# Performance work log

Measured on AMD Instinct MI355X. Metric: run time of the kernel, lower is better.

The kernel has to match this reference:

```python
import jax, jax.numpy as jnp
import numpy as np

DIM = 1024
NUM_HEADS = 8
HEAD_DIM = 128
MAX_SEQ_LEN = 2048
ATTN_SCALE = 0.12
RMS_EPS = 1.1920929e-07  # torch float32 eps (F.rms_norm default)


def rms_norm(x):
    return x * jax.lax.rsqrt(jnp.mean(jnp.square(x), axis=-1, keepdims=True) + RMS_EPS)


def rope_tables(T):
    # angular_freq: (1/1024)**linspace(0,1,head_dim//4), padded with head_dim//4 zeros -> length head_dim//2
    af = (1.0 / 1024.0) ** np.linspace(0.0, 1.0, HEAD_DIM // 4, dtype=np.float32)
    af = np.concatenate([af, np.zeros(HEAD_DIM // 4, dtype=np.float32)])
    t = np.arange(T, dtype=np.float32)
    theta = np.einsum('i,j->ij', t, af)  # [T, head_dim//2]
    return jnp.asarray(np.cos(theta)), jnp.asarray(np.sin(theta))


def apply_rope(x_BTHD, cos, sin):
    # cos/sin: [T, head_dim//2] -> broadcast [1,T,1,hd//2]
    c = cos[None, :, None, :]
    s = sin[None, :, None, :]
    x1, x2 = jnp.split(x_BTHD, 2, axis=-1)
    y1 = x1 * c + x2 * s
    y2 = -x1 * s + x2 * c
    return jnp.concatenate([y1, y2], axis=-1)


def setup_inputs() -> dict:
    key = jax.random.key(0)
    k1, k2, k3, k4, k5 = jax.random.split(key, 5)
    B, T = 4, 2048
    hdim = NUM_HEADS * HEAD_DIM
    std = 0.5 * DIM ** (-0.5)
    bound = (3.0 ** 0.5) * std
    x = jax.random.normal(k1, (B, T, DIM), dtype=jnp.float32)
    ve = jax.random.normal(k2, (B, T, DIM), dtype=jnp.float32)
    sa_lambdas = jax.random.uniform(k3, (2,), dtype=jnp.float32)
    qkv_w = jax.random.uniform(k4, (3, hdim, DIM), dtype=jnp.float32, minval=-bound, maxval=bound)
    # original inits c_proj to zeros; use small random so the output is non-trivial
    c_proj_weight = jax.random.normal(k5, (DIM, hdim), dtype=jnp.float32) * 0.02
    return {"x": x, "ve": ve, "sa_lambdas": sa_lambdas, "qkv_w": qkv_w,
            "c_proj_weight": c_proj_weight}


def reference(x, ve, sa_lambdas, qkv_w, c_proj_weight):
    B, T, D = x.shape
    H, hd = NUM_HEADS, HEAD_DIM
    Wqkv = qkv_w.reshape(3 * H * hd, D)
    qkv = jnp.einsum('btd,ed->bte', x, Wqkv).reshape(B, T, 3 * H, hd)
    q, k, v = jnp.split(qkv, 3, axis=-2)  # each [B,T,H,hd]
    q, k = rms_norm(q), rms_norm(k)
    cos, sin = rope_tables(T)
    q, k = apply_rope(q, cos, sin), apply_rope(k, cos, sin)
    v = sa_lambdas[0] * v + sa_lambdas[1] * ve.reshape(B, T, H, hd)
    # [B,H,T,T] scores
    attn = jnp.einsum('bqhd,bkhd->bhqk', q, k) * ATTN_SCALE
    causal = jnp.triu(jnp.ones((T, T), dtype=bool), k=1)
    attn = jnp.where(causal[None, None], -jnp.inf, attn)
    attn = jax.nn.softmax(attn, axis=-1)
    y = jnp.einsum('bhqk,bkhd->bqhd', attn, v).reshape(B, T, H * hd)
    return jnp.einsum('bte,de->btd', y, c_proj_weight)
```

## Files before the change

kernel.cpp:

```cpp
#include <hip/hip_runtime.h>

#define DIM 1024
#define NH 8
#define HD 128
#define T_SEQ 2048
#define NTOK 8192
#define QKV_N 3072
#define ATTN_SCALE 0.12f
#define RMS_EPS 1.1920929e-07f

using f32x4  = __attribute__((ext_vector_type(4))) float;
using bf16x8 = __attribute__((ext_vector_type(8))) __bf16;

__device__ __forceinline__ unsigned short f2bf(float f) {
    unsigned int u = __builtin_bit_cast(unsigned int, f);
    u += 0x7fffu + ((u >> 16) & 1u);
    return (unsigned short)(u >> 16);
}
__device__ __forceinline__ float bf2f(unsigned short s) {
    unsigned int u = ((unsigned int)s) << 16;
    return __builtin_bit_cast(float, u);
}
__device__ __forceinline__ unsigned int cvtpk(float lo, float hi) {
    unsigned int r;
    asm("v_cvt_pk_bf16_f32 %0, %1, %2" : "=v"(r) : "v"(lo), "v"(hi));
    return r;
}

__device__ __forceinline__ void gll16(const void* g, void* l) {
    __builtin_amdgcn_global_load_lds(
        (const __attribute__((address_space(1))) unsigned int*)g,
        (__attribute__((address_space(3))) unsigned int*)l, 16, 0, 0);
}

#define VMCNT(n) asm volatile("s_waitcnt vmcnt(" #n ")" ::: "memory")

__global__ __launch_bounds__(256) void cvt_f32_bf16(const float* __restrict__ in,
                                                    unsigned short* __restrict__ out,
                                                    int n4) {
    int i = blockIdx.x * 256 + threadIdx.x;
    if (i < n4) {
        float4 f = ((const float4*)in)[i];
        ushort4 o;
        o.x = f2bf(f.x); o.y = f2bf(f.y); o.z = f2bf(f.z); o.w = f2bf(f.w);
        ((ushort4*)out)[i] = o;
    }
}

__global__ __launch_bounds__(256) void rope_tab(float2* __restrict__ tab) {
    int idx = blockIdx.x * 256 + threadIdx.x;
    int t = idx >> 5, i = idx & 31;
    float th = (float)t * exp2f((float)i * (-10.0f/31.0f));
    float sn, cs;
    sincosf(th, &sn, &cs);
    tab[idx] = make_float2(cs, sn);
}

#define SLOT_A 32768
#define SLOT_SZ 49152

template<int OUTF32>
__global__ __launch_bounds__(512, 1) void gemm256(const unsigned short* __restrict__ A,
                                                  const unsigned short* __restrict__ B,
                                                  void* __restrict__ Cout,
                                                  int M, int N, int K, int nbn) {
    __shared__ __align__(16) char smem[147456];
    const int tid  = threadIdx.x;
    const int lane = tid & 63;
    const int w    = tid >> 6;
    const int wm   = w >> 1, wn = w & 1;
    const int lr   = lane & 15, lg = lane >> 4;
    const int xsw  = (lr & 7) << 3;

    const int chunk = gridDim.x >> 3;
    const int bid2  = (blockIdx.x & 7) * chunk + (blockIdx.x >> 3);
    const int m0 = (bid2 / nbn) * 256;
    const int n0 = (bid2 % nbn) * 128;

    const int rsub = lane >> 3;
    const int csw  = ((lane & 7) ^ rsub) << 3;

    char* s0 = smem;
    char* s1 = smem + SLOT_SZ;
    char* s2 = smem + 2*SLOT_SZ;

    auto stage = [&](int kt, char* slot) {
        const int kb = kt * 64;
        #pragma unroll
        for (int i = 0; i < 4; ++i) {
            int c = w*4 + i;
            gll16(&A[(size_t)(m0 + c*8 + rsub)*K + kb + csw], slot + c*1024);
        }
        #pragma unroll
        for (int i = 0; i < 2; ++i) {
            int c = w*2 + i;
            gll16(&B[(size_t)(n0 + c*8 + rsub)*K + kb + csw], slot + SLOT_A + c*1024);
        }
    };

    f32x4 acc[4][4] = {};
    const int KT = K / 64;

    stage(0, s0);
    stage(1, s1);
    VMCNT(6);
    __builtin_amdgcn_s_barrier();
    __builtin_amdgcn_sched_barrier(0);

    for (int t = 0; t < KT; ++t) {
        if (t + 2 < KT) stage(t + 2, s2);
        const unsigned short* sA = (const unsigned short*)s0;
        const unsigned short* sB = (const unsigned short*)(s0 + SLOT_A);
        bf16x8 bfr[4][2];
        #pragma unroll
        for (int n = 0; n < 4; ++n)
            #pragma unroll
            for (int kk = 0; kk < 2; ++kk)
                bfr[n][kk] = *(const bf16x8*)&sB[(wn*64 + n*16 + lr)*64 + ((kk*32 + lg*8) ^ xsw)];
        #pragma unroll
        for (int m = 0; m < 4; ++m) {
            bf16x8 af[2];
            #pragma unroll
            for (int kk = 0; kk < 2; ++kk)
                af[kk] = *(const bf16x8*)&sA[(wm*64 + m*16 + lr)*64 + ((kk*32 + lg*8) ^ xsw)];
            __builtin_amdgcn_s_setprio(1);
            #pragma unroll
            for (int n = 0; n < 4; ++n)
                #pragma unroll
                for (int kk = 0; kk < 2; ++kk)
                    acc[m][n] = __builtin_amdgcn_mfma_f32_16x16x32_bf16(af[kk], bfr[n][kk], acc[m][n], 0, 0, 0);
            __builtin_amdgcn_s_setprio(0);
        }
        if (t + 2 < KT) { VMCNT(6); }
        else            { VMCNT(0); }
        __builtin_amdgcn_s_barrier();
        __builtin_amdgcn_sched_barrier(0);
        char* tmp = s0; s0 = s1; s1 = s2; s2 = tmp;
    }

    __syncthreads();
    float* sc = (float*)(smem + (size_t)w * 17408);
    #pragma unroll
    for (int m = 0; m < 4; ++m)
        #pragma unroll
        for (int n = 0; n < 4; ++n)
            #pragma unroll
            for (int r = 0; r < 4; ++r)
                sc[(m*16 + lg*4 + r)*68 + n*16 + lr] = acc[m][n][r];

    if (OUTF32) {
        float* C = (float*)Cout;
        #pragma unroll
        for (int rnd = 0; rnd < 16; ++rnd) {
            int g = rnd*64 + lane;
            int row = g >> 4, c4 = (g & 15) * 4;
            float4 v = *(float4*)&sc[row*68 + c4];
            *(float4*)&C[(size_t)(m0 + wm*64 + row)*N + n0 + wn*64 + c4] = v;
        }
    } else {
        unsigned short* C = (unsigned short*)Cout;
        #pragma unroll
        for (int rnd = 0; rnd < 8; ++rnd) {
            int g = rnd*64 + lane;
            int row = g >> 3, c8 = (g & 7) * 8;
            float4 v0 = *(float4*)&sc[row*68 + c8];
            float4 v1 = *(float4*)&sc[row*68 + c8 + 4];
            uint4 o;
            o.x = f2bf(v0.x) | ((unsigned)f2bf(v0.y) << 16);
            o.y = f2bf(v0.z) | ((unsigned)f2bf(v0.w) << 16);
            o.z = f2bf(v1.x) | ((unsigned)f2bf(v1.y) << 16);
            o.w = f2bf(v1.z) | ((unsigned)f2bf(v1.w) << 16);
            *(uint4*)&C[(size_t)(m0 + wm*64 + row)*N + n0 + wn*64 + c8] = o;
        }
    }
}

__global__ __launch_bounds__(256) void qkv_post(const unsigned short* __restrict__ qkv,
                                                const float2* __restrict__ tab,
                                                unsigned short* __restrict__ qO,
                                                unsigned short* __restrict__ kO) {
    int gw   = (blockIdx.x * 256 + threadIdx.x) >> 6;
    int lane = threadIdx.x & 63;
    int h     = gw & 7;
    int token = gw >> 3;
    int t     = token & (T_SEQ-1);
    int b     = token >> 11;

    const unsigned short* base = qkv + (size_t)token * QKV_N + h*HD;
    float q1 = bf2f(base[lane]),        q2 = bf2f(base[lane+64]);
    float k1 = bf2f(base[1024+lane]),   k2 = bf2f(base[1024+lane+64]);

    float sq = q1*q1 + q2*q2;
    float sk = k1*k1 + k2*k2;
    #pragma unroll
    for (int m = 1; m < 64; m <<= 1) {
        sq += __shfl_xor(sq, m);
        sk += __shfl_xor(sk, m);
    }
    float qs = rsqrtf(sq * (1.0f/128.0f) + RMS_EPS) * (ATTN_SCALE * 1.44269504088896f);
    float ks = rsqrtf(sk * (1.0f/128.0f) + RMS_EPS);
    q1 *= qs; q2 *= qs; k1 *= ks; k2 *= ks;

    float cs = 1.0f, sn = 0.0f;
    if (lane < 32) { float2 cc = tab[t*32 + lane]; cs = cc.x; sn = cc.y; }
    float qy1 =  q1*cs + q2*sn, qy2 = -q1*sn + q2*cs;
    float ky1 =  k1*cs + k2*sn, ky2 = -k1*sn + k2*cs;

    size_t obase = ((size_t)(b*NH + h) * T_SEQ + t) * HD;
    qO[obase + lane]      = f2bf(qy1);
    qO[obase + lane + 64] = f2bf(qy2);
    kO[obase + lane]      = f2bf(ky1);
    kO[obase + lane + 64] = f2bf(ky2);
}

__global__ __launch_bounds__(256) void vmix_t(const unsigned short* __restrict__ qkv,
                                              const float* __restrict__ ve,
                                              const float* __restrict__ lam,
                                              unsigned short* __restrict__ vt) {
    __shared__ unsigned short lT[128*72];
    const int tid = threadIdx.x;
    const int t0  = blockIdx.x * 64;
    const int bh  = blockIdx.y;
    const int b = bh >> 3, h = bh & 7;
    const float l0 = lam[0], l1 = lam[1];

    #pragma unroll
    for (int it = 0; it < 4; ++it) {
        int g  = it*256 + tid;
        int t  = g >> 4;
        int d8 = (g & 15) << 3;
        size_t token = (size_t)b*T_SEQ + t0 + t;
        ushort4 v0 = *(const ushort4*)&qkv[token*QKV_N + 2048 + h*HD + d8];
        ushort4 v1 = *(const ushort4*)&qkv[token*QKV_N + 2048 + h*HD + d8 + 4];
        float4 e0 = *(const float4*)&ve[token*DIM + h*HD + d8];
        float4 e1 = *(const float4*)&ve[token*DIM + h*HD + d8 + 4];
        lT[(d8+0)*72 + t] = f2bf(l0*bf2f(v0.x) + l1*e0.x);
        lT[(d8+1)*72 + t] = f2bf(l0*bf2f(v0.y) + l1*e0.y);
        lT[(d8+2)*72 + t] = f2bf(l0*bf2f(v0.z) + l1*e0.z);
        lT[(d8+3)*72 + t] = f2bf(l0*bf2f(v0.w) + l1*e0.w);
        lT[(d8+4)*72 + t] = f2bf(l0*bf2f(v1.x) + l1*e1.x);
        lT[(d8+5)*72 + t] = f2bf(l0*bf2f(v1.y) + l1*e1.y);
        lT[(d8+6)*72 + t] = f2bf(l0*bf2f(v1.z) + l1*e1.z);
        lT[(d8+7)*72 + t] = f2bf(l0*bf2f(v1.w) + l1*e1.w);
    }
    __syncthreads();
    #pragma unroll
    for (int it = 0; it < 4; ++it) {
        int g  = it*256 + tid;
        int d  = g >> 3;
        int t8 = (g & 7) << 3;
        uint4 pk = *(const uint4*)&lT[d*72 + t8];
        *(uint4*)&vt[((size_t)bh*HD + d)*T_SEQ + t0 + t8] = pk;
    }
}

__global__ __launch_bounds__(256, 2) void attn_fwd(const unsigned short* __restrict__ Q,
                                                   const unsigned short* __restrict__ K,
                                                   const unsigned short* __restrict__ Vt,
                                                   unsigned short* __restrict__ Y) {
    __shared__ unsigned short lK[2][64*128];
    __shared__ unsigned short lV[2][128*64];
    __shared__ unsigned short lP[4][16*72];
    __shared__ float lden[4][2][16];

    const int tid  = threadIdx.x;
    const int lane = tid & 63;
    const int w    = tid >> 6;
    const int lr   = lane & 15, lg = lane >> 4;

    const int lin = blockIdx.y * 16 + blockIdx.x;
    const int bh  = (lin & 7)*4 + ((lin >> 3) & 3);
    const int p   = lin >> 5;
    const int qtA = p, qtB = 31 - p;

    const unsigned short* Qg = Q  + (size_t)bh * T_SEQ * HD;
    const unsigned short* Kg = K  + (size_t)bh * T_SEQ * HD;
    const unsigned short* Vg = Vt + (size_t)bh * HD * T_SEQ;
    const int q0A = qtA*64 + w*16;
    const int q0B = qtB*64 + w*16;

    auto stage = [&](int kt, int s) {
        const int kbase = kt * 64;
        #pragma unroll
        for (int i = 0; i < 4; ++i) {
            int c = w*4 + i;
            int row = c*4 + (lane >> 4);
            int col = ((lane & 15) << 3) ^ ((row & 7) << 3);
            gll16(&Kg[(size_t)(kbase + row)*HD + col], &lK[s][c*512]);
        }
        #pragma unroll
        for (int i = 0; i < 4; ++i) {
            int c = w*4 + i;
            int row = c*8 + (lane >> 3);
            int col = ((lane & 7) << 3) ^ ((row & 7) << 3);
            gll16(&Vg[(size_t)row*T_SEQ + kbase + col], &lV[s][c*512]);
        }
    };

    bf16x8 qfA[4], qfB[4];
    #pragma unroll
    for (int kk = 0; kk < 4; ++kk) {
        qfA[kk] = *(const bf16x8*)&Qg[(size_t)(q0A + lr)*HD + kk*32 + lg*8];
        qfB[kk] = *(const bf16x8*)&Qg[(size_t)(q0B + lr)*HD + kk*32 + lg*8];
    }
    VMCNT(0);
    #pragma unroll
    for (int kk = 0; kk < 4; ++kk)
        asm volatile("" :: "v"(qfA[kk]), "v"(qfB[kk]));

    f32x4 oA[8] = {}, oB[8] = {};
    float psA = 0.f, psB = 0.f;

    auto pass = [&](const bf16x8* qf, f32x4* o, float& ps, int q0, bool diag,
                    int kbase, const unsigned short* lKc, const unsigned short* lVc) {
        f32x4 sf[4];
        __builtin_amdgcn_s_setprio(1);
        #pragma unroll
        for (int j = 0; j < 4; ++j) {
            f32x4 s = {0.f,0.f,0.f,0.f};
            #pragma unroll
            for (int kk = 0; kk < 4; ++kk) {
                bf16x8 kf = *(const bf16x8*)&lKc[(j*16+lr)*128 + ((kk*32 + lg*8) ^ ((lr&7)<<3))];
                s = __builtin_amdgcn_mfma_f32_16x16x32_bf16(kf, qf[kk], s, 0, 0, 0);
            }
            sf[j] = s;
        }
        __builtin_amdgcn_s_setprio(0);
        if (diag) {
            #pragma unroll
            for (int j = 0; j < 4; ++j)
                #pragma unroll
                for (int r = 0; r < 4; ++r) {
                    int kcol = kbase + j*16 + lg*4 + r;
                    int qrow = q0 + lr;
                    if (kcol > qrow) sf[j][r] = -INFINITY;
                }
        }
        #pragma unroll
        for (int j = 0; j < 4; ++j)
            #pragma unroll
            for (int r = 0; r < 4; ++r) {
                float pp = exp2f(sf[j][r]);
                sf[j][r] = pp;
                ps += pp;
            }
        asm volatile("" ::: "memory");
        #pragma unroll
        for (int j = 0; j < 4; ++j) {
            uint2 pk;
            pk.x = cvtpk(sf[j][0], sf[j][1]);
            pk.y = cvtpk(sf[j][2], sf[j][3]);
            *(uint2*)&lP[w][lr*72 + j*16 + lg*4] = pk;
        }
        asm volatile("" ::: "memory");
        bf16x8 pf[2];
        #pragma unroll
        for (int kk = 0; kk < 2; ++kk)
            pf[kk] = *(const bf16x8*)&lP[w][lr*72 + kk*32 + lg*8];
        #pragma unroll
        for (int n = 0; n < 8; ++n) {
            bf16x8 vf0 = *(const bf16x8*)&lVc[(n*16+lr)*64 + (( 0 + lg*8) ^ ((lr&7)<<3))];
            bf16x8 vf1 = *(const bf16x8*)&lVc[(n*16+lr)*64 + ((32 + lg*8) ^ ((lr&7)<<3))];
            __builtin_amdgcn_s_setprio(1);
            o[n] = __builtin_amdgcn_mfma_f32_16x16x32_bf16(pf[0], vf0, o[n], 0, 0, 0);
            o[n] = __builtin_amdgcn_mfma_f32_16x16x32_bf16(pf[1], vf1, o[n], 0, 0, 0);
            __builtin_amdgcn_s_setprio(0);
        }
    };

    stage(0, 0);
    for (int kt = 0; kt <= qtB; ++kt) {
        __builtin_amdgcn_s_barrier();
        const bool pre = (kt + 1 <= qtB);
        if (pre) stage(kt + 1, (kt + 1) & 1);
        if (pre) { VMCNT(8); } else { VMCNT(0); }
        __builtin_amdgcn_sched_barrier(0);
        const int kbase = kt * 64;
        const unsigned short* lKc = lK[kt & 1];
        const unsigned short* lVc = lV[kt & 1];
        if (kt <= qtA) pass(qfA, oA, psA, q0A, kt == qtA, kbase, lKc, lVc);
        pass(qfB, oB, psB, q0B, kt == qtB, kbase, lKc, lVc);
    }

    psA += __shfl_xor(psA, 16); psA += __shfl_xor(psA, 32);
    psB += __shfl_xor(psB, 16); psB += __shfl_xor(psB, 32);
    if (lane < 16) { lden[w][0][lane] = psA; lden[w][1][lane] = psB; }
    asm volatile("" ::: "memory");
    float riA[4], riB[4];
    #pragma unroll
    for (int r = 0; r < 4; ++r) {
        riA[r] = 1.0f / lden[w][0][lg*4 + r];
        riB[r] = 1.0f / lden[w][1][lg*4 + r];
    }

    const int b = bh >> 3, h = bh & 7;
    #pragma unroll
    for (int n = 0; n < 8; ++n)
        #pragma unroll
        for (int r = 0; r < 4; ++r) {
            int d = n*16 + lr;
            int qrowA = q0A + lg*4 + r;
            int qrowB = q0B + lg*4 + r;
            Y[((size_t)(b*T_SEQ + qrowA))*DIM + h*HD + d] = f2bf(oA[n][r] * riA[r]);
            Y[((size_t)(b*T_SEQ + qrowB))*DIM + h*HD + d] = f2bf(oB[n][r] * riB[r]);
        }
}

extern "C" void kernel_launch(void* const* d_in, const int* in_sizes, int n_in,
                              void* d_out, int out_size, void* d_ws, size_t ws_size,
                              hipStream_t stream) {
    const float* x      = (const float*)d_in[0];
    const float* ve     = (const float*)d_in[1];
    const float* lam    = (const float*)d_in[2];
    const float* qkvw   = (const float*)d_in[3];
    const float* cprojw = (const float*)d_in[4];

    char* ws = (char*)d_ws;
    unsigned short* xb  = (unsigned short*)(ws);
    unsigned short* wqb = (unsigned short*)(ws + 16777216);
    unsigned short* cpb = (unsigned short*)(ws + 23068672);
    unsigned short* qkv = (unsigned short*)(ws + 25165824);
    unsigned short* qa  = (unsigned short*)(ws + 75497472);
    unsigned short* ka  = (unsigned short*)(ws + 92274688);
    unsigned short* vt  = (unsigned short*)(ws + 109051904);
    unsigned short* ya  = (unsigned short*)(ws + 125829120);
    float2* tab = (float2*)(ws);

    cvt_f32_bf16<<<8192, 256, 0, stream>>>(x, xb, 2097152);
    cvt_f32_bf16<<<3072, 256, 0, stream>>>(qkvw, wqb, 786432);
    cvt_f32_bf16<<<1024, 256, 0, stream>>>(cprojw, cpb, 262144);

    gemm256<0><<<768, 512, 0, stream>>>(xb, wqb, qkv, NTOK, QKV_N, DIM, 24);
    rope_tab<<<256, 256, 0, stream>>>(tab);
    qkv_post<<<16384, 256, 0, stream>>>(qkv, tab, qa, ka);
    vmix_t<<<dim3(32, 32), 256, 0, stream>>>(qkv, ve, lam, vt);
    attn_fwd<<<dim3(16, 32), 256, 0, stream>>>(qa, ka, vt, ya);
    gemm256<1><<<256, 512, 0, stream>>>(ya, cpb, (float*)d_out, NTOK, DIM, DIM, 8);
}
```

Baseline: 199.5 us.

## Merge prep kernels into one launch and share K/V fragments across two query tiles

```diff
diff --git a/kernel.cpp b/kernel.cpp
--- a/kernel.cpp
+++ b/kernel.cpp
@@ -35,25 +35,34 @@
 
 #define VMCNT(n) asm volatile("s_waitcnt vmcnt(" #n ")" ::: "memory")
 
-__global__ __launch_bounds__(256) void cvt_f32_bf16(const float* __restrict__ in,
-                                                    unsigned short* __restrict__ out,
-                                                    int n4) {
-    int i = blockIdx.x * 256 + threadIdx.x;
-    if (i < n4) {
+__global__ __launch_bounds__(256) void prep(const float* __restrict__ x,
+                                            const float* __restrict__ qkvw,
+                                            const float* __restrict__ cprojw,
+                                            unsigned short* __restrict__ xb,
+                                            unsigned short* __restrict__ wqb,
+                                            unsigned short* __restrict__ cpb,
+                                            float2* __restrict__ tab) {
+    const int bid = blockIdx.x;
+    const int tid = threadIdx.x;
+    if (bid < 12288) {
+        const float* in;
+        unsigned short* out;
+        int i;
+        if (bid < 8192)        { in = x;      out = xb;  i = bid*256 + tid; }
+        else if (bid < 11264)  { in = qkvw;   out = wqb; i = (bid-8192)*256 + tid; }
+        else                   { in = cprojw; out = cpb; i = (bid-11264)*256 + tid; }
         float4 f = ((const float4*)in)[i];
         ushort4 o;
         o.x = f2bf(f.x); o.y = f2bf(f.y); o.z = f2bf(f.z); o.w = f2bf(f.w);
         ((ushort4*)out)[i] = o;
-    }
-}
-
-__global__ __launch_bounds__(256) void rope_tab(float2* __restrict__ tab) {
-    int idx = blockIdx.x * 256 + threadIdx.x;
-    int t = idx >> 5, i = idx & 31;
-    float th = (float)t * exp2f((float)i * (-10.0f/31.0f));
-    float sn, cs;
-    sincosf(th, &sn, &cs);
-    tab[idx] = make_float2(cs, sn);
+    } else {
+        int idx = (bid - 12288)*256 + tid;
+        int t = idx >> 5, i = idx & 31;
+        float th = (float)t * exp2f((float)i * (-10.0f/31.0f));
+        float sn, cs;
+        sincosf(th, &sn, &cs);
+        tab[idx] = make_float2(cs, sn);
+    }
 }
 
 #define SLOT_A 32768
@@ -311,31 +320,7 @@
     f32x4 oA[8] = {}, oB[8] = {};
     float psA = 0.f, psB = 0.f;
 
-    auto pass = [&](const bf16x8* qf, f32x4* o, float& ps, int q0, bool diag,
-                    int kbase, const unsigned short* lKc, const unsigned short* lVc) {
-        f32x4 sf[4];
-        __builtin_amdgcn_s_setprio(1);
-        #pragma unroll
-        for (int j = 0; j < 4; ++j) {
-            f32x4 s = {0.f,0.f,0.f,0.f};
-            #pragma unroll
-            for (int kk = 0; kk < 4; ++kk) {
-                bf16x8 kf = *(const bf16x8*)&lKc[(j*16+lr)*128 + ((kk*32 + lg*8) ^ ((lr&7)<<3))];
-                s = __builtin_amdgcn_mfma_f32_16x16x32_bf16(kf, qf[kk], s, 0, 0, 0);
-            }
-            sf[j] = s;
-        }
-        __builtin_amdgcn_s_setprio(0);
-        if (diag) {
-            #pragma unroll
-            for (int j = 0; j < 4; ++j)
-                #pragma unroll
-                for (int r = 0; r < 4; ++r) {
-                    int kcol = kbase + j*16 + lg*4 + r;
-                    int qrow = q0 + lr;
-                    if (kcol > qrow) sf[j][r] = -INFINITY;
-                }
-        }
+    auto softmax_store = [&](f32x4* sf, float& ps) {
         #pragma unroll
         for (int j = 0; j < 4; ++j)
             #pragma unroll
@@ -344,7 +329,6 @@
                 sf[j][r] = pp;
                 ps += pp;
             }
-        asm volatile("" ::: "memory");
         #pragma unroll
         for (int j = 0; j < 4; ++j) {
             uint2 pk;
@@ -353,17 +337,95 @@
             *(uint2*)&lP[w][lr*72 + j*16 + lg*4] = pk;
         }
         asm volatile("" ::: "memory");
-        bf16x8 pf[2];
+    };
+
+    auto passAB = [&](bool diagA, int kbase,
+                      const unsigned short* lKc, const unsigned short* lVc) {
+        f32x4 sfA[4], sfB[4];
+        __builtin_amdgcn_s_setprio(1);
+        #pragma unroll
+        for (int j = 0; j < 4; ++j) {
+            f32x4 sA = {0.f,0.f,0.f,0.f}, sB = {0.f,0.f,0.f,0.f};
+            #pragma unroll
+            for (int kk = 0; kk < 4; ++kk) {
+                bf16x8 kf = *(const bf16x8*)&lKc[(j*16+lr)*128 + ((kk*32 + lg*8) ^ ((lr&7)<<3))];
+                sA = __builtin_amdgcn_mfma_f32_16x16x32_bf16(kf, qfA[kk], sA, 0, 0, 0);
+                sB = __builtin_amdgcn_mfma_f32_16x16x32_bf16(kf, qfB[kk], sB, 0, 0, 0);
+            }
+            sfA[j] = sA; sfB[j] = sB;
+        }
+        __builtin_amdgcn_s_setprio(0);
+        if (diagA) {
+            #pragma unroll
+            for (int j = 0; j < 4; ++j)
+                #pragma unroll
+                for (int r = 0; r < 4; ++r) {
+                    int kcol = kbase + j*16 + lg*4 + r;
+                    int qrow = q0A + lr;
+                    if (kcol > qrow) sfA[j][r] = -INFINITY;
+                }
+        }
+        softmax_store(sfA, psA);
+        bf16x8 pfA[2];
         #pragma unroll
         for (int kk = 0; kk < 2; ++kk)
-            pf[kk] = *(const bf16x8*)&lP[w][lr*72 + kk*32 + lg*8];
+            pfA[kk] = *(const bf16x8*)&lP[w][lr*72 + kk*32 + lg*8];
+        asm volatile("" ::: "memory");
+        softmax_store(sfB, psB);
+        bf16x8 pfB[2];
+        #pragma unroll
+        for (int kk = 0; kk < 2; ++kk)
+            pfB[kk] = *(const bf16x8*)&lP[w][lr*72 + kk*32 + lg*8];
         #pragma unroll
         for (int n = 0; n < 8; ++n) {
             bf16x8 vf0 = *(const bf16x8*)&lVc[(n*16+lr)*64 + (( 0 + lg*8) ^ ((lr&7)<<3))];
             bf16x8 vf1 = *(const bf16x8*)&lVc[(n*16+lr)*64 + ((32 + lg*8) ^ ((lr&7)<<3))];
             __builtin_amdgcn_s_setprio(1);
-            o[n] = __builtin_amdgcn_mfma_f32_16x16x32_bf16(pf[0], vf0, o[n], 0, 0, 0);
-            o[n] = __builtin_amdgcn_mfma_f32_16x16x32_bf16(pf[1], vf1, o[n], 0, 0, 0);
+            oA[n] = __builtin_amdgcn_mfma_f32_16x16x32_bf16(pfA[0], vf0, oA[n], 0, 0, 0);
+            oB[n] = __builtin_amdgcn_mfma_f32_16x16x32_bf16(pfB[0], vf0, oB[n], 0, 0, 0);
+            oA[n] = __builtin_amdgcn_mfma_f32_16x16x32_bf16(pfA[1], vf1, oA[n], 0, 0, 0);
+            oB[n] = __builtin_amdgcn_mfma_f32_16x16x32_bf16(pfB[1], vf1, oB[n], 0, 0, 0);
+            __builtin_amdgcn_s_setprio(0);
+        }
+    };
+
+    auto pass = [&](bool diag, int kbase,
+                    const unsigned short* lKc, const unsigned short* lVc) {
+        f32x4 sf[4];
+        __builtin_amdgcn_s_setprio(1);
+        #pragma unroll
+        for (int j = 0; j < 4; ++j) {
+            f32x4 s = {0.f,0.f,0.f,0.f};
+            #pragma unroll
+            for (int kk = 0; kk < 4; ++kk) {
+                bf16x8 kf = *(const bf16x8*)&lKc[(j*16+lr)*128 + ((kk*32 + lg*8) ^ ((lr&7)<<3))];
+                s = __builtin_amdgcn_mfma_f32_16x16x32_bf16(kf, qfB[kk], s, 0, 0, 0);
+            }
+            sf[j] = s;
+        }
+        __builtin_amdgcn_s_setprio(0);
+        if (diag) {
+            #pragma unroll
+            for (int j = 0; j < 4; ++j)
+                #pragma unroll
+                for (int r = 0; r < 4; ++r) {
+                    int kcol = kbase + j*16 + lg*4 + r;
+                    int qrow = q0B + lr;
+                    if (kcol > qrow) sf[j][r] = -INFINITY;
+                }
+        }
+        softmax_store(sf, psB);
+        bf16x8 pf[2];
+        #pragma unroll
+        for (int kk = 0; kk < 2; ++kk)
+            pf[kk] = *(const bf16x8*)&lP[w][lr*72 + kk*32 + lg*8];
+        #pragma unroll
+        for (int n = 0; n < 8; ++n) {
+            bf16x8 vf0 = *(const bf16x8*)&lVc[(n*16+lr)*64 + (( 0 + lg*8) ^ ((lr&7)<<3))];
+            bf16x8 vf1 = *(const bf16x8*)&lVc[(n*16+lr)*64 + ((32 + lg*8) ^ ((lr&7)<<3))];
+            __builtin_amdgcn_s_setprio(1);
+            oB[n] = __builtin_amdgcn_mfma_f32_16x16x32_bf16(pf[0], vf0, oB[n], 0, 0, 0);
+            oB[n] = __builtin_amdgcn_mfma_f32_16x16x32_bf16(pf[1], vf1, oB[n], 0, 0, 0);
             __builtin_amdgcn_s_setprio(0);
         }
     };
@@ -378,8 +440,8 @@
         const int kbase = kt * 64;
         const unsigned short* lKc = lK[kt & 1];
         const unsigned short* lVc = lV[kt & 1];
-        if (kt <= qtA) pass(qfA, oA, psA, q0A, kt == qtA, kbase, lKc, lVc);
-        pass(qfB, oB, psB, q0B, kt == qtB, kbase, lKc, lVc);
+        if (kt <= qtA) passAB(kt == qtA, kbase, lKc, lVc);
+        else           pass(kt == qtB, kbase, lKc, lVc);
     }
 
     psA += __shfl_xor(psA, 16); psA += __shfl_xor(psA, 32);
@@ -424,14 +486,11 @@
     unsigned short* ka  = (unsigned short*)(ws + 92274688);
     unsigned short* vt  = (unsigned short*)(ws + 109051904);
     unsigned short* ya  = (unsigned short*)(ws + 125829120);
-    float2* tab = (float2*)(ws);
-
-    cvt_f32_bf16<<<8192, 256, 0, stream>>>(x, xb, 2097152);
-    cvt_f32_bf16<<<3072, 256, 0, stream>>>(qkvw, wqb, 786432);
-    cvt_f32_bf16<<<1024, 256, 0, stream>>>(cprojw, cpb, 262144);
+    float2* tab = (float2*)(ws + 142606336);
+
+    prep<<<12544, 256, 0, stream>>>(x, qkvw, cprojw, xb, wqb, cpb, tab);
 
     gemm256<0><<<768, 512, 0, stream>>>(xb, wqb, qkv, NTOK, QKV_N, DIM, 24);
-    rope_tab<<<256, 256, 0, stream>>>(tab);
     qkv_post<<<16384, 256, 0, stream>>>(qkv, tab, qa, ka);
     vmix_t<<<dim3(32, 32), 256, 0, stream>>>(qkv, ve, lam, vt);
     attn_fwd<<<dim3(16, 32), 256, 0, stream>>>(qa, ka, vt, ya);
```

Result: faster. 195.4 us (-2.1%).
